# Kernel optimization log

Hardware: AMD Instinct MI355X
Metric: run time of the kernel (lower is better)

## Reference

```python
import jax, jax.numpy as jnp
import numpy as np

N_HEADS = 8
HEAD_DIM = 64  # hidden_dim 512 / 8 heads
EPS = 1e-12    # F.normalize clamp_min eps


def setup_inputs() -> dict:
    key = jax.random.key(0)
    k1, k2, k3, k4 = jax.random.split(key, 4)
    B, C, H, W = 2, 256, 48, 48
    hidden = N_HEADS * HEAD_DIM
    x = jax.random.normal(k1, (B, C, H, W), dtype=jnp.float32)
    w_qkv = jax.random.normal(k2, (hidden * 3, C), dtype=jnp.float32) * 0.02
    w_proj = jax.random.normal(k3, (C, hidden), dtype=jnp.float32) * 0.02
    b_proj = jax.random.normal(k4, (C,), dtype=jnp.float32) * 0.02
    return {"x": x, "w_qkv": w_qkv, "w_proj": w_proj, "b_proj": b_proj}


def _l2norm_tokens(t):
    # normalize along the token axis (last dim), matching F.normalize(dim=-1)
    n = jnp.sqrt(jnp.sum(t * t, axis=-1, keepdims=True))
    return t / jnp.maximum(n, EPS)


def reference(x, w_qkv, w_proj, b_proj):
    B, C, H, W = x.shape
    N = H * W
    # 1x1 conv == channel matmul
    qkv = jnp.einsum('oc,bchw->bohw', w_qkv, x)  # [B, 3*hidden, H, W]
    qkv = qkv.reshape(B, 3, N_HEADS, HEAD_DIM, N)
    q, k, v = qkv[:, 0], qkv[:, 1], qkv[:, 2]    # each [B, h, d, N]
    q = _l2norm_tokens(q)
    k = _l2norm_tokens(k)
    # attn = q^T @ k over head_dim -> [B, h, N, N]; note: qk_scale unused in source
    attn = jnp.einsum('bhdn,bhdm->bhnm', q, k)
    attn = jax.nn.softmax(attn, axis=-1)
    # out = attn @ v^T -> [B, h, N, d], then permute to [B, h, d, N]
    out = jnp.einsum('bhnm,bhdm->bhdn', attn, v)
    out = out.reshape(B, N_HEADS * HEAD_DIM, H, W)
    # proj 1x1 conv with bias
    y = jnp.einsum('oc,bchw->bohw', w_proj, out) + b_proj[None, :, None, None]
    return y
```

## Files before the change

### kernel.cpp

```cpp
#include <hip/hip_runtime.h>
#include <math.h>

#define NTOK 2304
#define BATCH 2
#define CIN 256
#define HID 512
#define NH 8
#define LOG2E 1.44269504088896340736f

typedef __attribute__((ext_vector_type(8))) short bfrag;
typedef __attribute__((ext_vector_type(16))) float f32x16;

#if __has_builtin(__builtin_amdgcn_exp2f)
#define EXP2(x) __builtin_amdgcn_exp2f(x)
#else
#define EXP2(x) exp2f(x)
#endif

__device__ __forceinline__ unsigned f2bf(float f) {
    unsigned u = __float_as_uint(f);
    u += 0x7FFF + ((u >> 16) & 1);
    return u >> 16;
}

__device__ __forceinline__ unsigned pk_trunc(float a, float b) {
    return __builtin_amdgcn_perm(__float_as_uint(b), __float_as_uint(a), 0x07060302u);
}

__device__ __forceinline__ void softmax_frag(
    const f32x16& accS, int h, float& ps0, float& ps1, bfrag& P0, bfrag& P1)
{
    unsigned dw[8];
#pragma unroll
    for (int i = 0; i < 8; i++) {
        float plo = EXP2(accS[2 * i]);
        float phi = EXP2(accS[2 * i + 1]);
        dw[i] = pk_trunc(plo, phi);
        ps0 += __uint_as_float(dw[i] << 16);
        ps1 += __uint_as_float(dw[i] & 0xffff0000u);
    }
    unsigned sa0 = h ? dw[0] : dw[2], sb0 = h ? dw[1] : dw[3];
    unsigned sa1 = h ? dw[4] : dw[6], sb1 = h ? dw[5] : dw[7];
    unsigned ra0 = (unsigned)__shfl_xor((int)sa0, 32, 64);
    unsigned rb0 = (unsigned)__shfl_xor((int)sb0, 32, 64);
    unsigned ra1 = (unsigned)__shfl_xor((int)sa1, 32, 64);
    unsigned rb1 = (unsigned)__shfl_xor((int)sb1, 32, 64);
    union { bfrag f; unsigned u[4]; } U0, U1;
    U0.u[0] = h ? ra0 : dw[0];  U0.u[1] = h ? rb0 : dw[1];
    U0.u[2] = h ? dw[2] : ra0;  U0.u[3] = h ? dw[3] : rb0;
    U1.u[0] = h ? ra1 : dw[4];  U1.u[1] = h ? rb1 : dw[5];
    U1.u[2] = h ? dw[6] : ra1;  U1.u[3] = h ? dw[7] : rb1;
    P0 = U0.f; P1 = U1.f;
}

__global__ __launch_bounds__(256) void pack_weights(
    const float* __restrict__ wq, short* __restrict__ wqb,
    const float* __restrict__ wp, short* __restrict__ wpb)
{
    int e = (blockIdx.x * 256 + threadIdx.x) * 8;
    const int NQ = 1536 * 256;
    const float* src; short* dst;
    if (e < NQ) { src = wq + e; dst = wqb + e; }
    else        { src = wp + (e - NQ); dst = wpb + (e - NQ); }
    float4 v0 = ((const float4*)src)[0];
    float4 v1 = ((const float4*)src)[1];
    unsigned b0 = f2bf(v0.x) | (f2bf(v0.y) << 16);
    unsigned b1 = f2bf(v0.z) | (f2bf(v0.w) << 16);
    unsigned b2 = f2bf(v1.x) | (f2bf(v1.y) << 16);
    unsigned b3 = f2bf(v1.z) | (f2bf(v1.w) << 16);
    *((uint4*)dst) = make_uint4(b0, b1, b2, b3);
}

__global__ __launch_bounds__(256) void pack_xT(
    const float* __restrict__ x, short* __restrict__ xT)
{
    int n0 = blockIdx.x * 64, c0 = blockIdx.y * 64, b = blockIdx.z;
    __shared__ float sT[64][65];
    int tid = threadIdx.x, lane = tid & 63, wv = tid >> 6;
    for (int c = wv; c < 64; c += 4)
        sT[c][lane] = x[((size_t)b * CIN + c0 + c) * NTOK + n0 + lane];
    __syncthreads();
    int n = tid >> 2, c4 = (tid & 3) * 16;
    unsigned buf[8];
#pragma unroll
    for (int i = 0; i < 8; i++)
        buf[i] = f2bf(sT[c4 + 2 * i][n]) | (f2bf(sT[c4 + 2 * i + 1][n]) << 16);
    short* dst = xT + ((size_t)b * NTOK + n0 + n) * CIN + c0 + c4;
    ((uint4*)dst)[0] = make_uint4(buf[0], buf[1], buf[2], buf[3]);
    ((uint4*)dst)[1] = make_uint4(buf[4], buf[5], buf[6], buf[7]);
}

__global__ __launch_bounds__(256, 2) void gemm_qkv(
    const short* __restrict__ A, const short* __restrict__ B,
    float* __restrict__ qkf, short* __restrict__ vb)
{
    const int K = CIN;
    int b = blockIdx.z;
    int o0 = blockIdx.y * 128;
    int n0 = blockIdx.x * 128;
    int tid = threadIdx.x, wv = tid >> 6, lane = tid & 63;
    int h = lane >> 5, l31 = lane & 31;

    const short* pa = A + (size_t)(o0 + l31) * K + h * 8;
    const short* pb = B + ((size_t)b * NTOK + n0 + wv * 32 + l31) * K + h * 8;

    f32x16 acc[4];
#pragma unroll
    for (int rb = 0; rb < 4; rb++)
#pragma unroll
        for (int r = 0; r < 16; r++) acc[rb][r] = 0.f;

#pragma unroll 2
    for (int kt = 0; kt < K; kt += 16) {
        bfrag a0 = *(const bfrag*)(pa + kt);
        bfrag a1 = *(const bfrag*)(pa + (size_t)32 * K + kt);
        bfrag a2 = *(const bfrag*)(pa + (size_t)64 * K + kt);
        bfrag a3 = *(const bfrag*)(pa + (size_t)96 * K + kt);
        bfrag bb = *(const bfrag*)(pb + kt);
        acc[0] = __builtin_amdgcn_mfma_f32_32x32x16_bf16(a0, bb, acc[0], 0, 0, 0);
        acc[1] = __builtin_amdgcn_mfma_f32_32x32x16_bf16(a1, bb, acc[1], 0, 0, 0);
        acc[2] = __builtin_amdgcn_mfma_f32_32x32x16_bf16(a2, bb, acc[2], 0, 0, 0);
        acc[3] = __builtin_amdgcn_mfma_f32_32x32x16_bf16(a3, bb, acc[3], 0, 0, 0);
    }

    int nn = n0 + wv * 32 + l31;
    if (o0 < 1024) {
        float* Q = qkf + (size_t)b * 1024 * NTOK;
#pragma unroll
        for (int rb = 0; rb < 4; rb++)
#pragma unroll
            for (int r = 0; r < 16; r++) {
                int ml = (r & 3) + 8 * (r >> 2) + 4 * h;
                Q[(size_t)(o0 + rb * 32 + ml) * NTOK + nn] = acc[rb][r];
            }
    } else {
        short* V = vb + (size_t)b * 512 * NTOK;
        int ov = o0 - 1024;
        int mb = nn >> 5, jc = (nn >> 4) & 1, hv = (nn >> 3) & 1, e = nn & 7;
#pragma unroll
        for (int rb = 0; rb < 4; rb++)
#pragma unroll
            for (int r = 0; r < 16; r++) {
                int ml = (r & 3) + 8 * (r >> 2) + 4 * h;
                int row = ov + rb * 32 + ml;
                int hh2 = row >> 6, dl = row & 63;
                int jr = dl >> 5, l31v = dl & 31;
                V[((((size_t)hh2 * 72 + mb) * 4 + jr * 2 + jc) * 64
                   + hv * 32 + l31v) * 8 + e] = (short)f2bf(acc[rb][r]);
            }
    }
}

__global__ __launch_bounds__(256) void rownorm(
    const float* __restrict__ qkf, float* __restrict__ invn)
{
    int row = blockIdx.x;
    int b = row >> 10, o = row & 1023;
    const float* p = qkf + ((size_t)b * 1024 + o) * NTOK;
    int tid = threadIdx.x;
    float s = 0.f;
    for (int n = tid; n < NTOK; n += 256) { float v = p[n]; s += v * v; }
#pragma unroll
    for (int off = 32; off > 0; off >>= 1) s += __shfl_down(s, off, 64);
    __shared__ float ws[4];
    if ((tid & 63) == 0) ws[tid >> 6] = s;
    __syncthreads();
    if (tid == 0) {
        float tot = ws[0] + ws[1] + ws[2] + ws[3];
        invn[row] = 1.f / fmaxf(sqrtf(tot), 1e-12f);
    }
}

__global__ __launch_bounds__(256) void pack_qk(
    const float* __restrict__ qkf, const float* __restrict__ invn,
    short* __restrict__ qkt)
{
    int n0 = blockIdx.x * 64;
    int bh = blockIdx.y;
    int sel = blockIdx.z;
    int b = bh >> 3, h = bh & 7;
    const float* src = qkf + ((size_t)b * 1024 + sel * 512 + h * 64) * NTOK;
    int base = b * 1024 + sel * 512 + h * 64;
    float extra = sel == 0 ? LOG2E : 1.f;

    __shared__ float sT[64][65];
    int tid = threadIdx.x, lane = tid & 63, wv = tid >> 6;
    for (int d = wv; d < 64; d += 4)
        sT[d][lane] = src[(size_t)d * NTOK + n0 + lane] * (invn[base + d] * extra);
    __syncthreads();

    int n = tid >> 2, c4 = (tid & 3) * 16;
    unsigned buf[8];
#pragma unroll
    for (int i = 0; i < 8; i++)
        buf[i] = f2bf(sT[c4 + 2 * i][n]) | (f2bf(sT[c4 + 2 * i + 1][n]) << 16);
    int t = n0 + n;
    int mb = t >> 5, l31 = t & 31, fi = c4 >> 4;
    short* dst = qkt + (size_t)sel * ((size_t)16 * NTOK * 64)
               + (size_t)bh * NTOK * 64
               + ((size_t)mb * 4 + fi) * 512;
    ((uint4*)(dst + (0 * 32 + l31) * 8))[0] = make_uint4(buf[0], buf[1], buf[2], buf[3]);
    ((uint4*)(dst + (1 * 32 + l31) * 8))[0] = make_uint4(buf[4], buf[5], buf[6], buf[7]);
}

__global__ __launch_bounds__(256, 4) void attn_nb(
    const short* __restrict__ qkt,
    const short* __restrict__ vb,
    float* __restrict__ Opart,
    float* __restrict__ lsum)
{
    int bid = blockIdx.x;
    int g = bid & 31;
    int bh = g >> 1, ms = g & 1;
    int ntile = bid >> 5;
    int b = bh >> 3, hh = bh & 7;
    int tid = threadIdx.x, wv = tid >> 6, lane = tid & 63;
    int h = lane >> 5, l31 = lane & 31;
    int nb = ntile * 128 + wv * 32;
    int mb0 = ms * 36;

    const short* Qt = qkt + (size_t)bh * NTOK * 64;
    const short* kp = qkt + (size_t)16 * NTOK * 64 + (size_t)bh * NTOK * 64
                    + ((size_t)mb0 * 4) * 512 + lane * 8;
    const short* vp = vb + (((size_t)(b * 8 + hh) * 72 + mb0) * 4) * 512 + lane * 8;

    bfrag bQ[4];
    {
        const short* q0 = Qt + ((size_t)(nb >> 5) * 4) * 512 + lane * 8;
#pragma unroll
        for (int i = 0; i < 4; i++) bQ[i] = *(const bfrag*)(q0 + i * 512);
    }

    f32x16 aL, aH;
#pragma unroll
    for (int r = 0; r < 16; r++) { aL[r] = 0.f; aH[r] = 0.f; }
    float s0 = 0.f, s1 = 0.f;

    bfrag ck[4], cv[4];
#pragma unroll
    for (int i = 0; i < 4; i++) {
        ck[i] = *(const bfrag*)(kp + i * 512);
        cv[i] = *(const bfrag*)(vp + i * 512);
    }

#pragma unroll 2
    for (int it = 0; it < 36; it++) {
        kp += 2048; vp += 2048;
        bfrag nk[4], nv[4];
#pragma unroll
        for (int i = 0; i < 4; i++) {
            nk[i] = *(const bfrag*)(kp + i * 512);
            nv[i] = *(const bfrag*)(vp + i * 512);
        }

        bfrag P0, P1;
        {
            f32x16 accS;
#pragma unroll
            for (int r = 0; r < 16; r++) accS[r] = 0.f;
            accS = __builtin_amdgcn_mfma_f32_32x32x16_bf16(ck[0], bQ[0], accS, 0, 0, 0);
            accS = __builtin_amdgcn_mfma_f32_32x32x16_bf16(ck[1], bQ[1], accS, 0, 0, 0);
            accS = __builtin_amdgcn_mfma_f32_32x32x16_bf16(ck[2], bQ[2], accS, 0, 0, 0);
            accS = __builtin_amdgcn_mfma_f32_32x32x16_bf16(ck[3], bQ[3], accS, 0, 0, 0);
            softmax_frag(accS, h, s0, s1, P0, P1);
        }
        aL = __builtin_amdgcn_mfma_f32_32x32x16_bf16(P0, cv[0], aL, 0, 0, 0);
        aL = __builtin_amdgcn_mfma_f32_32x32x16_bf16(P1, cv[1], aL, 0, 0, 0);
        aH = __builtin_amdgcn_mfma_f32_32x32x16_bf16(P0, cv[2], aH, 0, 0, 0);
        aH = __builtin_amdgcn_mfma_f32_32x32x16_bf16(P1, cv[3], aH, 0, 0, 0);

#pragma unroll
        for (int i = 0; i < 4; i++) { ck[i] = nk[i]; cv[i] = nv[i]; }
    }

    float p0 = s0 + s1;
    p0 += __shfl_xor(p0, 32, 64);
    if (h == 0)
        lsum[((size_t)ms * 16 + bh) * NTOK + nb + l31] = p0;

    float* Ob = Opart + (size_t)ms * (2ull * NTOK * HID)
              + (size_t)b * NTOK * HID + hh * 64;
#pragma unroll
    for (int r = 0; r < 16; r++) {
        int ml = (r & 3) + 8 * (r >> 2) + 4 * h;
        Ob[(size_t)(nb + ml) * HID + l31] = aL[r];
        Ob[(size_t)(nb + ml) * HID + 32 + l31] = aH[r];
    }
}

__global__ __launch_bounds__(256) void combine(
    const float* __restrict__ Opart, const float* __restrict__ lsum,
    short* __restrict__ aoT)
{
    size_t e = ((size_t)blockIdx.x * 256 + threadIdx.x) * 8;
    int c = (int)(e & 511);
    size_t row = e >> 9;
    int b = (int)(row / NTOK), n = (int)(row - (size_t)b * NTOK);
    int hh = c >> 6;
    float l0 = lsum[(size_t)(b * 8 + hh) * NTOK + n];
    float l1 = lsum[(size_t)16 * NTOK + (size_t)(b * 8 + hh) * NTOK + n];
    float inv = 1.f / (l0 + l1);
    const float* P0 = Opart + e;
    const float* P1 = Opart + (size_t)2 * NTOK * HID + e;
    float4 a0 = ((const float4*)P0)[0], a1 = ((const float4*)P0)[1];
    float4 c0 = ((const float4*)P1)[0], c1 = ((const float4*)P1)[1];
    unsigned b0 = f2bf((a0.x + c0.x) * inv) | (f2bf((a0.y + c0.y) * inv) << 16);
    unsigned b1 = f2bf((a0.z + c0.z) * inv) | (f2bf((a0.w + c0.w) * inv) << 16);
    unsigned b2 = f2bf((a1.x + c1.x) * inv) | (f2bf((a1.y + c1.y) * inv) << 16);
    unsigned b3 = f2bf((a1.z + c1.z) * inv) | (f2bf((a1.w + c1.w) * inv) << 16);
    *((uint4*)(aoT + e)) = make_uint4(b0, b1, b2, b3);
}

__global__ __launch_bounds__(256, 2) void gemm_proj(
    const short* __restrict__ A, const short* __restrict__ B,
    const float* __restrict__ bias, float* __restrict__ y)
{
    const int K = HID;
    int b = blockIdx.z;
    int o0 = blockIdx.y * 64;
    int n0 = blockIdx.x * 128;
    int tid = threadIdx.x, wv = tid >> 6, lane = tid & 63;
    int h = lane >> 5, l31 = lane & 31;

    const short* pa0 = A + (size_t)(o0 + l31) * K + h * 8;
    const short* pa1 = pa0 + (size_t)32 * K;
    const short* pb  = B + ((size_t)b * NTOK + n0 + wv * 32 + l31) * K + h * 8;

    f32x16 acc0, acc1;
#pragma unroll
    for (int r = 0; r < 16; r++) { acc0[r] = 0.f; acc1[r] = 0.f; }

#pragma unroll 4
    for (int kt = 0; kt < K; kt += 16) {
        bfrag a0 = *(const bfrag*)(pa0 + kt);
        bfrag a1 = *(const bfrag*)(pa1 + kt);
        bfrag bb = *(const bfrag*)(pb + kt);
        acc0 = __builtin_amdgcn_mfma_f32_32x32x16_bf16(a0, bb, acc0, 0, 0, 0);
        acc1 = __builtin_amdgcn_mfma_f32_32x32x16_bf16(a1, bb, acc1, 0, 0, 0);
    }

    int nn = n0 + wv * 32 + l31;
#pragma unroll
    for (int r = 0; r < 16; r++) {
        int ml = (r & 3) + 8 * (r >> 2) + 4 * h;
        y[((size_t)b * CIN + o0 + ml) * NTOK + nn] = acc0[r] + bias[o0 + ml];
        y[((size_t)b * CIN + o0 + 32 + ml) * NTOK + nn] = acc1[r] + bias[o0 + 32 + ml];
    }
}

extern "C" void kernel_launch(void* const* d_in, const int* in_sizes, int n_in,
                              void* d_out, int out_size, void* d_ws, size_t ws_size,
                              hipStream_t stream)
{
    const float* x      = (const float*)d_in[0];
    const float* w_qkv  = (const float*)d_in[1];
    const float* w_proj = (const float*)d_in[2];
    const float* b_proj = (const float*)d_in[3];
    float* y = (float*)d_out;

    float* qkf   = (float*)d_ws;
    float* Opart = (float*)d_ws;
    short* vb    = (short*)((char*)d_ws + 18874368);
    short* qkt   = (short*)((char*)d_ws + 23592960);
    short* aoT   = (short*)((char*)d_ws + 23592960);
    float* lsum  = (float*)((char*)d_ws + 33030144);
    short* xT    = (short*)((char*)d_ws + 33030144);
    short* wqb   = (short*)((char*)d_ws + 35389440);
    short* wpb   = (short*)((char*)d_ws + 36175872);
    float* invn  = (float*)((char*)d_ws + 36438016);

    pack_weights<<<(1536 * 256 + 256 * 512) / 8 / 256, 256, 0, stream>>>(
        w_qkv, wqb, w_proj, wpb);
    pack_xT<<<dim3(NTOK / 64, CIN / 64, BATCH), 256, 0, stream>>>(x, xT);
    gemm_qkv<<<dim3(NTOK / 128, 1536 / 128, BATCH), 256, 0, stream>>>(
        wqb, xT, qkf, vb);
    rownorm<<<2048, 256, 0, stream>>>(qkf, invn);
    pack_qk<<<dim3(NTOK / 64, BATCH * NH, 2), 256, 0, stream>>>(qkf, invn, qkt);
    attn_nb<<<576, 256, 0, stream>>>(qkt, vb, Opart, lsum);
    combine<<<(BATCH * NTOK * HID / 8) / 256, 256, 0, stream>>>(Opart, lsum, aoT);
    gemm_proj<<<dim3(NTOK / 128, CIN / 64, BATCH), 256, 0, stream>>>(
        wpb, aoT, b_proj, y);
}
```

Before: 161.0 us.

## Pre-swizzle GEMM operands into MFMA fragment order for coalesced loads

```diff
diff --git a/kernel.cpp b/kernel.cpp
--- a/kernel.cpp
+++ b/kernel.cpp
@@ -60,8 +60,16 @@
     int e = (blockIdx.x * 256 + threadIdx.x) * 8;
     const int NQ = 1536 * 256;
     const float* src; short* dst;
-    if (e < NQ) { src = wq + e; dst = wqb + e; }
-    else        { src = wp + (e - NQ); dst = wpb + (e - NQ); }
+    if (e < NQ) {
+        int row = e >> 8, c = e & 255;
+        int off = (((row >> 5) * 16 + (c >> 4)) * 64 + ((c >> 3) & 1) * 32 + (row & 31)) * 8;
+        src = wq + e; dst = wqb + off;
+    } else {
+        int e2 = e - NQ;
+        int row = e2 >> 9, c = e2 & 511;
+        int off = (((row >> 5) * 32 + (c >> 4)) * 64 + ((c >> 3) & 1) * 32 + (row & 31)) * 8;
+        src = wp + e2; dst = wpb + off;
+    }
     float4 v0 = ((const float4*)src)[0];
     float4 v1 = ((const float4*)src)[1];
     unsigned b0 = f2bf(v0.x) | (f2bf(v0.y) << 16);
@@ -85,24 +93,26 @@
 #pragma unroll
     for (int i = 0; i < 8; i++)
         buf[i] = f2bf(sT[c4 + 2 * i][n]) | (f2bf(sT[c4 + 2 * i + 1][n]) << 16);
-    short* dst = xT + ((size_t)b * NTOK + n0 + n) * CIN + c0 + c4;
-    ((uint4*)dst)[0] = make_uint4(buf[0], buf[1], buf[2], buf[3]);
-    ((uint4*)dst)[1] = make_uint4(buf[4], buf[5], buf[6], buf[7]);
+    int n_tok = n0 + n;
+    int l31n = n & 31;
+    short* dst = xT + (((size_t)b * 72 + (n_tok >> 5)) * 16 + ((c0 + c4) >> 4)) * 512;
+    ((uint4*)(dst + (0 * 32 + l31n) * 8))[0] = make_uint4(buf[0], buf[1], buf[2], buf[3]);
+    ((uint4*)(dst + (1 * 32 + l31n) * 8))[0] = make_uint4(buf[4], buf[5], buf[6], buf[7]);
 }
 
 __global__ __launch_bounds__(256, 2) void gemm_qkv(
-    const short* __restrict__ A, const short* __restrict__ B,
+    const short* __restrict__ A,
+    const short* __restrict__ B,
     float* __restrict__ qkf, short* __restrict__ vb)
 {
-    const int K = CIN;
     int b = blockIdx.z;
     int o0 = blockIdx.y * 128;
     int n0 = blockIdx.x * 128;
     int tid = threadIdx.x, wv = tid >> 6, lane = tid & 63;
     int h = lane >> 5, l31 = lane & 31;
 
-    const short* pa = A + (size_t)(o0 + l31) * K + h * 8;
-    const short* pb = B + ((size_t)b * NTOK + n0 + wv * 32 + l31) * K + h * 8;
+    const short* pa = A + ((size_t)(o0 >> 5) * 16) * 512 + lane * 8;
+    const short* pb = B + (((size_t)b * 72 + (n0 >> 5) + wv) * 16) * 512 + lane * 8;
 
     f32x16 acc[4];
 #pragma unroll
@@ -111,12 +121,12 @@
         for (int r = 0; r < 16; r++) acc[rb][r] = 0.f;
 
 #pragma unroll 2
-    for (int kt = 0; kt < K; kt += 16) {
-        bfrag a0 = *(const bfrag*)(pa + kt);
-        bfrag a1 = *(const bfrag*)(pa + (size_t)32 * K + kt);
-        bfrag a2 = *(const bfrag*)(pa + (size_t)64 * K + kt);
-        bfrag a3 = *(const bfrag*)(pa + (size_t)96 * K + kt);
-        bfrag bb = *(const bfrag*)(pb + kt);
+    for (int kc = 0; kc < 16; kc++) {
+        bfrag a0 = *(const bfrag*)(pa + (size_t)(0 * 16 + kc) * 512);
+        bfrag a1 = *(const bfrag*)(pa + (size_t)(1 * 16 + kc) * 512);
+        bfrag a2 = *(const bfrag*)(pa + (size_t)(2 * 16 + kc) * 512);
+        bfrag a3 = *(const bfrag*)(pa + (size_t)(3 * 16 + kc) * 512);
+        bfrag bb = *(const bfrag*)(pb + (size_t)kc * 512);
         acc[0] = __builtin_amdgcn_mfma_f32_32x32x16_bf16(a0, bb, acc[0], 0, 0, 0);
         acc[1] = __builtin_amdgcn_mfma_f32_32x32x16_bf16(a1, bb, acc[1], 0, 0, 0);
         acc[2] = __builtin_amdgcn_mfma_f32_32x32x16_bf16(a2, bb, acc[2], 0, 0, 0);
@@ -292,49 +302,50 @@
     const float* __restrict__ Opart, const float* __restrict__ lsum,
     short* __restrict__ aoT)
 {
-    size_t e = ((size_t)blockIdx.x * 256 + threadIdx.x) * 8;
-    int c = (int)(e & 511);
-    size_t row = e >> 9;
-    int b = (int)(row / NTOK), n = (int)(row - (size_t)b * NTOK);
-    int hh = c >> 6;
+    int s = blockIdx.x * 256 + threadIdx.x;
+    int lane = s & 63, kc = (s >> 6) & 31, nbb = s >> 11;
+    int b = nbb >= 72 ? 1 : 0, nb = nbb - 72 * b;
+    int h = lane >> 5, l31 = lane & 31;
+    int n = nb * 32 + l31;
+    int k0 = kc * 16 + h * 8;
+    int hh = kc >> 2;
     float l0 = lsum[(size_t)(b * 8 + hh) * NTOK + n];
     float l1 = lsum[(size_t)16 * NTOK + (size_t)(b * 8 + hh) * NTOK + n];
     float inv = 1.f / (l0 + l1);
-    const float* P0 = Opart + e;
-    const float* P1 = Opart + (size_t)2 * NTOK * HID + e;
+    const float* P0 = Opart + ((size_t)b * NTOK + n) * HID + k0;
+    const float* P1 = P0 + (size_t)2 * NTOK * HID;
     float4 a0 = ((const float4*)P0)[0], a1 = ((const float4*)P0)[1];
     float4 c0 = ((const float4*)P1)[0], c1 = ((const float4*)P1)[1];
     unsigned b0 = f2bf((a0.x + c0.x) * inv) | (f2bf((a0.y + c0.y) * inv) << 16);
     unsigned b1 = f2bf((a0.z + c0.z) * inv) | (f2bf((a0.w + c0.w) * inv) << 16);
     unsigned b2 = f2bf((a1.x + c1.x) * inv) | (f2bf((a1.y + c1.y) * inv) << 16);
     unsigned b3 = f2bf((a1.z + c1.z) * inv) | (f2bf((a1.w + c1.w) * inv) << 16);
-    *((uint4*)(aoT + e)) = make_uint4(b0, b1, b2, b3);
+    *((uint4*)(aoT + (size_t)s * 8)) = make_uint4(b0, b1, b2, b3);
 }
 
 __global__ __launch_bounds__(256, 2) void gemm_proj(
-    const short* __restrict__ A, const short* __restrict__ B,
+    const short* __restrict__ A,
+    const short* __restrict__ B,
     const float* __restrict__ bias, float* __restrict__ y)
 {
-    const int K = HID;
     int b = blockIdx.z;
     int o0 = blockIdx.y * 64;
     int n0 = blockIdx.x * 128;
     int tid = threadIdx.x, wv = tid >> 6, lane = tid & 63;
     int h = lane >> 5, l31 = lane & 31;
 
-    const short* pa0 = A + (size_t)(o0 + l31) * K + h * 8;
-    const short* pa1 = pa0 + (size_t)32 * K;
-    const short* pb  = B + ((size_t)b * NTOK + n0 + wv * 32 + l31) * K + h * 8;
+    const short* pa = A + ((size_t)(o0 >> 5) * 32) * 512 + lane * 8;
+    const short* pb = B + (((size_t)b * 72 + (n0 >> 5) + wv) * 32) * 512 + lane * 8;
 
     f32x16 acc0, acc1;
 #pragma unroll
     for (int r = 0; r < 16; r++) { acc0[r] = 0.f; acc1[r] = 0.f; }
 
 #pragma unroll 4
-    for (int kt = 0; kt < K; kt += 16) {
-        bfrag a0 = *(const bfrag*)(pa0 + kt);
-        bfrag a1 = *(const bfrag*)(pa1 + kt);
-        bfrag bb = *(const bfrag*)(pb + kt);
+    for (int kc = 0; kc < 32; kc++) {
+        bfrag a0 = *(const bfrag*)(pa + (size_t)kc * 512);
+        bfrag a1 = *(const bfrag*)(pa + (size_t)(32 + kc) * 512);
+        bfrag bb = *(const bfrag*)(pb + (size_t)kc * 512);
         acc0 = __builtin_amdgcn_mfma_f32_32x32x16_bf16(a0, bb, acc0, 0, 0, 0);
         acc1 = __builtin_amdgcn_mfma_f32_32x32x16_bf16(a1, bb, acc1, 0, 0, 0);
     }
@@ -377,7 +388,7 @@
     rownorm<<<2048, 256, 0, stream>>>(qkf, invn);
     pack_qk<<<dim3(NTOK / 64, BATCH * NH, 2), 256, 0, stream>>>(qkf, invn, qkt);
     attn_nb<<<576, 256, 0, stream>>>(qkt, vb, Opart, lsum);
-    combine<<<(BATCH * NTOK * HID / 8) / 256, 256, 0, stream>>>(Opart, lsum, aoT);
+    combine<<<1152, 256, 0, stream>>>(Opart, lsum, aoT);
     gemm_proj<<<dim3(NTOK / 128, CIN / 64, BATCH), 256, 0, stream>>>(
         wpb, aoT, b_proj, y);
 }
```

Measured after the change: 147.5 us. 8.4% less time.
